# Kernel tuning notes

Hardware: AMD Instinct MI355X
Metric: run time of the kernel (lower is better)

The kernel has to match this reference:

```python
import jax, jax.numpy as jnp
import numpy as np

GAMMA = 1.0
N_EXPERTS = 16
K = 8                      # number of trees (units of every Dense)
DEPTH = 4                  # log2(N_EXPERTS)
B, D_IN, D_OUT = 8192, 1024, 1024


def smoothstep(v):
    # 0 if v<=-g/2 ; 1 if v>=g/2 ; -2/g^3 v^3 + 3/(2g) v + 0.5 otherwise
    g = GAMMA
    poly = (-2.0 / g**3) * v**3 + (3.0 / (2.0 * g)) * v + 0.5
    return jnp.where(v <= -g / 2, 0.0, jnp.where(v >= g / 2, 1.0, poly))


def setup_inputs() -> dict:
    key = jax.random.key(0)
    ks = jax.random.split(key, 7)
    f = jax.random.normal(ks[0], (B, D_OUT, N_EXPERTS), jnp.float32)   # stacked experts
    x = jax.random.normal(ks[1], (B, D_IN), jnp.float32)               # routing inputs
    permutation_weights = jax.random.uniform(ks[2], (K, N_EXPERTS, N_EXPERTS), jnp.float32)
    zlo, zhi = -GAMMA / 100, GAMMA / 100                               # z_initializer range
    Wz = jax.random.uniform(ks[3], (N_EXPERTS - 1, D_IN, K), jnp.float32, zlo, zhi)
    bz = jax.random.uniform(ks[4], (N_EXPERTS - 1, K), jnp.float32, zlo, zhi)
    Ww = jax.random.uniform(ks[5], (N_EXPERTS, D_IN, K), jnp.float32)  # w_initializer U(0,1)
    bw = jax.random.uniform(ks[6], (N_EXPERTS, K), jnp.float32)
    return {"f": f, "x": x, "permutation_weights": permutation_weights,
            "Wz": Wz, "bz": bz, "Ww": Ww, "bw": bw}


def reference(f, x, permutation_weights, Wz, bz, Ww, bw):
    b = x.shape[0]
    # selector activations for all internal nodes (BFS order): [B, N_EXPERTS-1, K]
    s = smoothstep(jnp.einsum('bd,ndk->bnk', x, Wz) + bz)
    # propagate path probabilities level by level down the complete binary tree
    prob = jnp.ones((b, 1, K), x.dtype)
    for level in range(DEPTH):
        start = 2**level - 1
        p = s[:, start:start + 2**level, :]               # [B, 2^level, K]
        # left child gets prob*p, right child gets prob*(1-p)
        prob = jnp.stack([prob * p, prob * (1.0 - p)], axis=2).reshape(b, 2**(level + 1), K)
    # leaf dense outputs: [B, N_EXPERTS, K]
    a = jnp.einsum('bd,ndk->bnk', x, Ww) + bw
    log_prob = jnp.where(prob <= 0.0, jnp.finfo(jnp.float32).min, jnp.log(prob + 1e-8))
    s_bj = jnp.swapaxes(a + log_prob, 1, 2)               # [B, K, N_EXPERTS] (leaf order)
    g = jax.nn.softmax(s_bj.reshape(b, K * N_EXPERTS), axis=-1)
    g = g.reshape(b, 1, K, N_EXPERTS)                     # [B, 1, K, N]
    g_perm = jnp.einsum('bijk,jkl->bijl', g, permutation_weights)
    g_perm = jnp.sum(g_perm, axis=2, keepdims=True)       # [B, 1, 1, N]
    g_perm = g_perm / jnp.sum(g_perm, axis=-1, keepdims=True)
    # y = sum_n f[:, :, n] * g[:, n]  -> [B, D_OUT]
    y = jnp.einsum('bdn,bn->bd', f, g_perm[:, 0, 0, :])
    return y
```

## Files before the change

kernel.cpp:

```cpp
#include <hip/hip_runtime.h>
#include <hip/hip_bf16.h>
#include <math.h>

#define B_ROWS 8192
#define D_IN 1024
#define D_OUT 1024
#define NEXP 16
#define KDIM 8
#define NCOL 256

__global__ void wt_pack_kernel(const float* __restrict__ Wz,
                               const float* __restrict__ Ww,
                               float* __restrict__ Wt) {
    int d = blockIdx.x;
    int col = threadIdx.x;
    float v = 0.0f;
    if (col < 120) {
        int n = col >> 3, k = col & 7;
        v = Wz[n * (D_IN * 8) + d * 8 + k];
    } else if (col < 248) {
        int c = col - 120;
        int n = c >> 3, k = c & 7;
        v = Ww[n * (D_IN * 8) + d * 8 + k];
    }
    Wt[d * NCOL + col] = v;
}

#define BM 64
#define BN 64
#define KC 16
__global__ __launch_bounds__(256) void gemm_kernel(const float* __restrict__ x,
                                                   const float* __restrict__ Wt,
                                                   float* __restrict__ ZA) {
    __shared__ float xs[KC][BM];
    __shared__ float wsh[KC][BN];

    const int tid = threadIdx.x;
    const int bRow = blockIdx.x;
    const int bCol = blockIdx.y;
    const int tr = tid >> 4;
    const int tc = tid & 15;

    const int lxRow = tid >> 2;
    const int lxK = (tid & 3) << 2;
    const int lwK = tid >> 4;
    const int lwC = (tid & 15) << 2;

    const float* xg = x + (bRow * BM + lxRow) * D_IN + lxK;
    const float* wg = Wt + lwK * NCOL + bCol * BN + lwC;

    float4 px = *(const float4*)xg;
    float4 pw = *(const float4*)wg;

    float acc[4][4];
#pragma unroll
    for (int i = 0; i < 4; ++i)
#pragma unroll
        for (int j = 0; j < 4; ++j) acc[i][j] = 0.0f;

    for (int kc = 0; kc < D_IN; kc += KC) {
        xs[lxK + 0][lxRow] = px.x;
        xs[lxK + 1][lxRow] = px.y;
        xs[lxK + 2][lxRow] = px.z;
        xs[lxK + 3][lxRow] = px.w;
        *(float4*)&wsh[lwK][lwC] = pw;
        __syncthreads();
        if (kc + KC < D_IN) {
            px = *(const float4*)(xg + kc + KC);
            pw = *(const float4*)(wg + (kc + KC) * NCOL);
        }
#pragma unroll
        for (int kk = 0; kk < KC; ++kk) {
            const float4 xa = *(const float4*)&xs[kk][tr << 2];
            const float4 wv = *(const float4*)&wsh[kk][tc << 2];
            const float xr[4] = {xa.x, xa.y, xa.z, xa.w};
            const float wc[4] = {wv.x, wv.y, wv.z, wv.w};
#pragma unroll
            for (int i = 0; i < 4; ++i)
#pragma unroll
                for (int j = 0; j < 4; ++j) acc[i][j] += xr[i] * wc[j];
        }
        __syncthreads();
    }

    const int row0 = bRow * BM + (tr << 2);
    const int col0 = bCol * BN + (tc << 2);
#pragma unroll
    for (int i = 0; i < 4; ++i) {
        float4 o;
        o.x = acc[i][0]; o.y = acc[i][1]; o.z = acc[i][2]; o.w = acc[i][3];
        *(float4*)&ZA[(row0 + i) * NCOL + col0] = o;
    }
}

__global__ __launch_bounds__(128) void gate_kernel(const float* __restrict__ ZA,
                                                   const float* __restrict__ bz,
                                                   const float* __restrict__ bw,
                                                   const float* __restrict__ perm,
                                                   float* __restrict__ wout) {
    __shared__ float red[128];
    __shared__ float u[128];

    const int b = blockIdx.x;
    const int tid = threadIdx.x;
    const int kk = tid >> 4;
    const int n = tid & 15;

    const float* za = ZA + b * NCOL;

    float prob = 1.0f;
#pragma unroll
    for (int L = 0; L < 4; ++L) {
        const int node = (1 << L) - 1 + (n >> (4 - L));
        const int bit = (n >> (3 - L)) & 1;
        const float v = za[node * 8 + kk] + bz[node * 8 + kk];
        float p;
        if (v <= -0.5f) p = 0.0f;
        else if (v >= 0.5f) p = 1.0f;
        else p = fmaf(-2.0f * v * v, v, fmaf(1.5f, v, 0.5f));
        prob *= bit ? (1.0f - p) : p;
    }

    const float a = za[120 + n * 8 + kk] + bw[n * 8 + kk];
    const float logit = (prob <= 0.0f) ? -3.4e38f : (a + logf(prob + 1e-8f));

    red[tid] = logit;
    __syncthreads();
#pragma unroll
    for (int s = 64; s > 0; s >>= 1) {
        if (tid < s) red[tid] = fmaxf(red[tid], red[tid + s]);
        __syncthreads();
    }
    const float mx = red[0];
    __syncthreads();

    u[tid] = expf(logit - mx);
    __syncthreads();

    const int l = tid & 15;
    const int chunk = tid >> 4;
    float partial = 0.0f;
#pragma unroll
    for (int e0 = 0; e0 < 16; ++e0) {
        const int e = chunk * 16 + e0;
        partial += u[e] * perm[(e >> 4) * 256 + (e & 15) * 16 + l];
    }
    red[tid] = partial;
    __syncthreads();
#pragma unroll
    for (int s = 64; s >= 16; s >>= 1) {
        if (tid < s) red[tid] += red[tid + s];
        __syncthreads();
    }
    if (tid < 16) {
        float tot = 0.0f;
#pragma unroll
        for (int l2 = 0; l2 < 16; ++l2) tot += red[l2];
        wout[b * NEXP + tid] = red[tid] / tot;
    }
}

__global__ __launch_bounds__(256) void out_kernel(const float* __restrict__ f,
                                                  const float* __restrict__ w,
                                                  float* __restrict__ y) {
    __shared__ float ws_[16];
    const int b = blockIdx.x >> 2;
    const int d = ((blockIdx.x & 3) << 8) + threadIdx.x;
    if (threadIdx.x < 16) ws_[threadIdx.x] = w[b * NEXP + threadIdx.x];
    __syncthreads();

    const long idx = (long)b * D_OUT + d;
    const float4* f4 = (const float4*)(f + idx * NEXP);
    const float4 a0 = f4[0];
    const float4 a1 = f4[1];
    const float4 a2 = f4[2];
    const float4 a3 = f4[3];

    float r = a0.x * ws_[0] + a0.y * ws_[1] + a0.z * ws_[2] + a0.w * ws_[3]
            + a1.x * ws_[4] + a1.y * ws_[5] + a1.z * ws_[6] + a1.w * ws_[7]
            + a2.x * ws_[8] + a2.y * ws_[9] + a2.z * ws_[10] + a2.w * ws_[11]
            + a3.x * ws_[12] + a3.y * ws_[13] + a3.z * ws_[14] + a3.w * ws_[15];
    y[idx] = r;
}

extern "C" void kernel_launch(void* const* d_in, const int* in_sizes, int n_in,
                              void* d_out, int out_size, void* d_ws, size_t ws_size,
                              hipStream_t stream) {
    const float* f = (const float*)d_in[0];
    const float* x = (const float*)d_in[1];
    const float* perm = (const float*)d_in[2];
    const float* Wz = (const float*)d_in[3];
    const float* bz = (const float*)d_in[4];
    const float* Ww = (const float*)d_in[5];
    const float* bw = (const float*)d_in[6];
    float* y = (float*)d_out;

    float* Wt = (float*)d_ws;
    float* ZA = Wt + D_IN * NCOL;
    float* Wexp = ZA + B_ROWS * NCOL;

    wt_pack_kernel<<<dim3(D_IN), dim3(NCOL), 0, stream>>>(Wz, Ww, Wt);
    gemm_kernel<<<dim3(B_ROWS / BM, NCOL / BN), dim3(256), 0, stream>>>(x, Wt, ZA);
    gate_kernel<<<dim3(B_ROWS), dim3(128), 0, stream>>>(ZA, bz, bw, perm, Wexp);
    out_kernel<<<dim3(B_ROWS * 4), dim3(256), 0, stream>>>(f, Wexp, y);
}
```

Baseline: 784.0 us.

## Fuse routing GEMM, gating softmax and expert combine into one kernel

Replaces the separate GEMM, gate and output kernels with a single kernel per 16-row tile. It computes the selector/leaf logits in registers, stores them in shared memory, runs the tree gating and softmax with wave shuffles, then streams f with nontemporal loads to produce y. This removes the ZA and gate-weight round trips through global memory and two launches. In exchange, every block re-reads the full packed weight matrix, and the bandwidth-bound f stream runs with only 512 blocks.

Result: slower. 890.9 us (+13.6%).

```diff
diff --git a/kernel.cpp b/kernel.cpp
--- a/kernel.cpp
+++ b/kernel.cpp
@@ -6,8 +6,11 @@
 #define D_IN 1024
 #define D_OUT 1024
 #define NEXP 16
-#define KDIM 8
 #define NCOL 256
+#define KC 16
+#define RTILE 16
+
+typedef float f32x4 __attribute__((ext_vector_type(4)));
 
 __global__ void wt_pack_kernel(const float* __restrict__ Wz,
                                const float* __restrict__ Ww,
@@ -26,31 +29,38 @@
     Wt[d * NCOL + col] = v;
 }
 
-#define BM 64
-#define BN 64
-#define KC 16
-__global__ __launch_bounds__(256) void gemm_kernel(const float* __restrict__ x,
-                                                   const float* __restrict__ Wt,
-                                                   float* __restrict__ ZA) {
-    __shared__ float xs[KC][BM];
-    __shared__ float wsh[KC][BN];
+__global__ __launch_bounds__(256) void fused_kernel(
+    const float* __restrict__ x,
+    const float* __restrict__ Wt,
+    const float* __restrict__ bz,
+    const float* __restrict__ bw,
+    const float* __restrict__ perm,
+    const float* __restrict__ f,
+    float* __restrict__ y)
+{
+    __shared__ float wsh[KC * NCOL];
+    __shared__ float xs[KC][RTILE];
+    __shared__ float perm_s[2048];
+    __shared__ float bz_s[120];
+    __shared__ float bw_s[128];
+    __shared__ float wexp_s[RTILE * 16];
 
     const int tid = threadIdx.x;
-    const int bRow = blockIdx.x;
-    const int bCol = blockIdx.y;
-    const int tr = tid >> 4;
-    const int tc = tid & 15;
-
-    const int lxRow = tid >> 2;
-    const int lxK = (tid & 3) << 2;
-    const int lwK = tid >> 4;
-    const int lwC = (tid & 15) << 2;
-
-    const float* xg = x + (bRow * BM + lxRow) * D_IN + lxK;
-    const float* wg = Wt + lwK * NCOL + bCol * BN + lwC;
-
-    float4 px = *(const float4*)xg;
-    float4 pw = *(const float4*)wg;
+    const int row0 = blockIdx.x * RTILE;
+
+    {
+        const float4* p4 = (const float4*)perm;
+        float4* s4 = (float4*)perm_s;
+        s4[tid] = p4[tid];
+        s4[256 + tid] = p4[256 + tid];
+        if (tid < 120) bz_s[tid] = bz[tid];
+        if (tid < 128) bw_s[tid] = bw[tid];
+    }
+
+    const int rg = tid >> 6;
+    const int cg = tid & 63;
+    const int sxRow = tid >> 2;
+    const int sxK = (tid & 3) << 2;
 
     float acc[4][4];
 #pragma unroll
@@ -58,129 +68,144 @@
 #pragma unroll
         for (int j = 0; j < 4; ++j) acc[i][j] = 0.0f;
 
+    float4 px, pw[4];
+    if (tid < 64) px = *(const float4*)&x[(row0 + sxRow) * D_IN + sxK];
+#pragma unroll
+    for (int j = 0; j < 4; ++j) {
+        const int flat = j * 256 + tid;
+        const int k = flat >> 6;
+        const int c4 = (flat & 63) << 2;
+        pw[j] = *(const float4*)&Wt[k * NCOL + c4];
+    }
+
     for (int kc = 0; kc < D_IN; kc += KC) {
-        xs[lxK + 0][lxRow] = px.x;
-        xs[lxK + 1][lxRow] = px.y;
-        xs[lxK + 2][lxRow] = px.z;
-        xs[lxK + 3][lxRow] = px.w;
-        *(float4*)&wsh[lwK][lwC] = pw;
+        if (tid < 64) {
+            xs[sxK + 0][sxRow] = px.x;
+            xs[sxK + 1][sxRow] = px.y;
+            xs[sxK + 2][sxRow] = px.z;
+            xs[sxK + 3][sxRow] = px.w;
+        }
+#pragma unroll
+        for (int j = 0; j < 4; ++j) {
+            const int flat = j * 256 + tid;
+            const int k = flat >> 6;
+            const int c4 = (flat & 63) << 2;
+            *(float4*)&wsh[k * NCOL + c4] = pw[j];
+        }
         __syncthreads();
         if (kc + KC < D_IN) {
-            px = *(const float4*)(xg + kc + KC);
-            pw = *(const float4*)(wg + (kc + KC) * NCOL);
+            if (tid < 64) px = *(const float4*)&x[(row0 + sxRow) * D_IN + kc + KC + sxK];
+#pragma unroll
+            for (int j = 0; j < 4; ++j) {
+                const int flat = j * 256 + tid;
+                const int k = flat >> 6;
+                const int c4 = (flat & 63) << 2;
+                pw[j] = *(const float4*)&Wt[(kc + KC + k) * NCOL + c4];
+            }
         }
 #pragma unroll
         for (int kk = 0; kk < KC; ++kk) {
-            const float4 xa = *(const float4*)&xs[kk][tr << 2];
-            const float4 wv = *(const float4*)&wsh[kk][tc << 2];
+            const float4 xa = *(const float4*)&xs[kk][rg << 2];
+            const float4 wv = *(const float4*)&wsh[kk * NCOL + (cg << 2)];
             const float xr[4] = {xa.x, xa.y, xa.z, xa.w};
             const float wc[4] = {wv.x, wv.y, wv.z, wv.w};
 #pragma unroll
             for (int i = 0; i < 4; ++i)
 #pragma unroll
-                for (int j = 0; j < 4; ++j) acc[i][j] += xr[i] * wc[j];
+                for (int j = 0; j < 4; ++j) acc[i][j] = fmaf(xr[i], wc[j], acc[i][j]);
         }
         __syncthreads();
     }
 
-    const int row0 = bRow * BM + (tr << 2);
-    const int col0 = bCol * BN + (tc << 2);
 #pragma unroll
     for (int i = 0; i < 4; ++i) {
         float4 o;
         o.x = acc[i][0]; o.y = acc[i][1]; o.z = acc[i][2]; o.w = acc[i][3];
-        *(float4*)&ZA[(row0 + i) * NCOL + col0] = o;
-    }
-}
-
-__global__ __launch_bounds__(128) void gate_kernel(const float* __restrict__ ZA,
-                                                   const float* __restrict__ bz,
-                                                   const float* __restrict__ bw,
-                                                   const float* __restrict__ perm,
-                                                   float* __restrict__ wout) {
-    __shared__ float red[128];
-    __shared__ float u[128];
-
-    const int b = blockIdx.x;
-    const int tid = threadIdx.x;
-    const int kk = tid >> 4;
-    const int n = tid & 15;
-
-    const float* za = ZA + b * NCOL;
-
-    float prob = 1.0f;
-#pragma unroll
-    for (int L = 0; L < 4; ++L) {
-        const int node = (1 << L) - 1 + (n >> (4 - L));
-        const int bit = (n >> (3 - L)) & 1;
-        const float v = za[node * 8 + kk] + bz[node * 8 + kk];
-        float p;
-        if (v <= -0.5f) p = 0.0f;
-        else if (v >= 0.5f) p = 1.0f;
-        else p = fmaf(-2.0f * v * v, v, fmaf(1.5f, v, 0.5f));
-        prob *= bit ? (1.0f - p) : p;
-    }
-
-    const float a = za[120 + n * 8 + kk] + bw[n * 8 + kk];
-    const float logit = (prob <= 0.0f) ? -3.4e38f : (a + logf(prob + 1e-8f));
-
-    red[tid] = logit;
+        *(float4*)&wsh[((rg << 2) + i) * NCOL + (cg << 2)] = o;
+    }
     __syncthreads();
-#pragma unroll
-    for (int s = 64; s > 0; s >>= 1) {
-        if (tid < s) red[tid] = fmaxf(red[tid], red[tid + s]);
-        __syncthreads();
-    }
-    const float mx = red[0];
+
+    {
+        const int gr = tid >> 4;
+        const int gn = tid & 15;
+        const float* za = &wsh[gr * NCOL];
+
+        float prob[8];
+#pragma unroll
+        for (int kk = 0; kk < 8; ++kk) prob[kk] = 1.0f;
+#pragma unroll
+        for (int L = 0; L < 4; ++L) {
+            const int node = (1 << L) - 1 + (gn >> (4 - L));
+            const int bit = (gn >> (3 - L)) & 1;
+#pragma unroll
+            for (int kk = 0; kk < 8; ++kk) {
+                const float v = za[node * 8 + kk] + bz_s[node * 8 + kk];
+                float p;
+                if (v <= -0.5f) p = 0.0f;
+                else if (v >= 0.5f) p = 1.0f;
+                else p = fmaf(-2.0f * v * v, v, fmaf(1.5f, v, 0.5f));
+                prob[kk] *= bit ? (1.0f - p) : p;
+            }
+        }
+        float logit[8];
+        float m = -3.4e38f;
+#pragma unroll
+        for (int kk = 0; kk < 8; ++kk) {
+            const float a = za[120 + gn * 8 + kk] + bw_s[gn * 8 + kk];
+            logit[kk] = (prob[kk] <= 0.0f) ? -3.4e38f : (a + logf(prob[kk] + 1e-8f));
+            m = fmaxf(m, logit[kk]);
+        }
+#pragma unroll
+        for (int s = 1; s < 16; s <<= 1) m = fmaxf(m, __shfl_xor(m, s, 16));
+
+        float u[8];
+#pragma unroll
+        for (int kk = 0; kk < 8; ++kk) u[kk] = expf(logit[kk] - m);
+
+        float part[16];
+#pragma unroll
+        for (int l = 0; l < 16; ++l) {
+            float s2 = 0.0f;
+#pragma unroll
+            for (int kk = 0; kk < 8; ++kk)
+                s2 = fmaf(u[kk], perm_s[kk * 256 + gn * 16 + l], s2);
+            part[l] = s2;
+        }
+#pragma unroll
+        for (int s = 1; s < 16; s <<= 1) {
+#pragma unroll
+            for (int l = 0; l < 16; ++l) part[l] += __shfl_xor(part[l], s, 16);
+        }
+        float tot = 0.0f;
+#pragma unroll
+        for (int l = 0; l < 16; ++l) tot += part[l];
+        wexp_s[gr * 16 + gn] = part[gn] / tot;
+    }
     __syncthreads();
 
-    u[tid] = expf(logit - mx);
-    __syncthreads();
-
-    const int l = tid & 15;
-    const int chunk = tid >> 4;
-    float partial = 0.0f;
-#pragma unroll
-    for (int e0 = 0; e0 < 16; ++e0) {
-        const int e = chunk * 16 + e0;
-        partial += u[e] * perm[(e >> 4) * 256 + (e & 15) * 16 + l];
-    }
-    red[tid] = partial;
-    __syncthreads();
-#pragma unroll
-    for (int s = 64; s >= 16; s >>= 1) {
-        if (tid < s) red[tid] += red[tid + s];
-        __syncthreads();
-    }
-    if (tid < 16) {
-        float tot = 0.0f;
-#pragma unroll
-        for (int l2 = 0; l2 < 16; ++l2) tot += red[l2];
-        wout[b * NEXP + tid] = red[tid] / tot;
-    }
-}
-
-__global__ __launch_bounds__(256) void out_kernel(const float* __restrict__ f,
-                                                  const float* __restrict__ w,
-                                                  float* __restrict__ y) {
-    __shared__ float ws_[16];
-    const int b = blockIdx.x >> 2;
-    const int d = ((blockIdx.x & 3) << 8) + threadIdx.x;
-    if (threadIdx.x < 16) ws_[threadIdx.x] = w[b * NEXP + threadIdx.x];
-    __syncthreads();
-
-    const long idx = (long)b * D_OUT + d;
-    const float4* f4 = (const float4*)(f + idx * NEXP);
-    const float4 a0 = f4[0];
-    const float4 a1 = f4[1];
-    const float4 a2 = f4[2];
-    const float4 a3 = f4[3];
-
-    float r = a0.x * ws_[0] + a0.y * ws_[1] + a0.z * ws_[2] + a0.w * ws_[3]
-            + a1.x * ws_[4] + a1.y * ws_[5] + a1.z * ws_[6] + a1.w * ws_[7]
-            + a2.x * ws_[8] + a2.y * ws_[9] + a2.z * ws_[10] + a2.w * ws_[11]
-            + a3.x * ws_[12] + a3.y * ws_[13] + a3.z * ws_[14] + a3.w * ws_[15];
-    y[idx] = r;
+    for (int r = 0; r < RTILE; ++r) {
+        const float4 w0 = *(const float4*)&wexp_s[r * 16 + 0];
+        const float4 w1 = *(const float4*)&wexp_s[r * 16 + 4];
+        const float4 w2 = *(const float4*)&wexp_s[r * 16 + 8];
+        const float4 w3 = *(const float4*)&wexp_s[r * 16 + 12];
+        const long grow = (long)(row0 + r);
+        const float* fbase = f + grow * D_OUT * NEXP;
+        float* ybase = y + grow * D_OUT;
+#pragma unroll
+        for (int c = 0; c < 4; ++c) {
+            const int d = c * 256 + tid;
+            const f32x4* f4 = (const f32x4*)(fbase + (long)d * NEXP);
+            const f32x4 a0 = __builtin_nontemporal_load(f4 + 0);
+            const f32x4 a1 = __builtin_nontemporal_load(f4 + 1);
+            const f32x4 a2 = __builtin_nontemporal_load(f4 + 2);
+            const f32x4 a3 = __builtin_nontemporal_load(f4 + 3);
+            float rsum = a0.x * w0.x + a0.y * w0.y + a0.z * w0.z + a0.w * w0.w
+                       + a1.x * w1.x + a1.y * w1.y + a1.z * w1.z + a1.w * w1.w
+                       + a2.x * w2.x + a2.y * w2.y + a2.z * w2.z + a2.w * w2.w
+                       + a3.x * w3.x + a3.y * w3.y + a3.z * w3.z + a3.w * w3.w;
+            __builtin_nontemporal_store(rsum, ybase + d);
+        }
+    }
 }
 
 extern "C" void kernel_launch(void* const* d_in, const int* in_sizes, int n_in,
@@ -196,11 +221,8 @@
     float* y = (float*)d_out;
 
     float* Wt = (float*)d_ws;
-    float* ZA = Wt + D_IN * NCOL;
-    float* Wexp = ZA + B_ROWS * NCOL;
 
     wt_pack_kernel<<<dim3(D_IN), dim3(NCOL), 0, stream>>>(Wz, Ww, Wt);
-    gemm_kernel<<<dim3(B_ROWS / BM, NCOL / BN), dim3(256), 0, stream>>>(x, Wt, ZA);
-    gate_kernel<<<dim3(B_ROWS), dim3(128), 0, stream>>>(ZA, bz, bw, perm, Wexp);
-    out_kernel<<<dim3(B_ROWS * 4), dim3(256), 0, stream>>>(f, Wexp, y);
+    fused_kernel<<<dim3(B_ROWS / RTILE), dim3(256), 0, stream>>>(
+        x, Wt, bz, bw, perm, f, y);
 }
```
